# Optimization experiments

Measured on AMD Instinct MI355X. Metric: run time of the kernel, lower is better.

The kernel has to match this reference:

```python
import math
import jax, jax.numpy as jnp
import numpy as np
from jax import lax

B, CIN, COUT, K, SDIM, H, W = 8, 64, 64, 3, 512, 256, 256
EPS = 1e-8

def setup_inputs() -> dict:
    key = jax.random.key(0)
    k1, k2, k3, k4 = jax.random.split(key, 4)
    return {
        "input": jax.random.normal(k1, (B, CIN, H, W), dtype=jnp.float32),
        "style": jax.random.normal(k2, (B, SDIM), dtype=jnp.float32),
        "weight": jax.random.normal(k3, (1, COUT, CIN, K, K), dtype=jnp.float32),
        "mod_weight": jax.random.normal(k4, (CIN, SDIM), dtype=jnp.float32),
        "mod_bias": jnp.ones((CIN,), dtype=jnp.float32),
    }

def reference(input, style, weight, mod_weight, mod_bias):
    b, cin, h, w = input.shape
    cout, k = weight.shape[1], weight.shape[3]
    scale = 1.0 / math.sqrt(cin * k * k)          # equalized-lr conv scale
    mod_scale = 1.0 / math.sqrt(mod_weight.shape[1])  # EqualLinear fan-in scale
    # style modulation: (B, Cin)
    s = jnp.einsum('bs,cs->bc', style, mod_weight) * mod_scale + mod_bias
    # modulated per-sample weights: (B, Cout, Cin, K, K)
    wmod = scale * weight * s[:, None, :, None, None]
    # demodulation over (Cin, K, K)
    demod = lax.rsqrt(jnp.sum(wmod * wmod, axis=(2, 3, 4)) + EPS)
    wmod = wmod * demod[:, :, None, None, None]
    # grouped conv with groups = batch
    x = input.reshape(1, b * cin, h, w)
    wg = wmod.reshape(b * cout, cin, k, k)
    pad = k // 2
    out = lax.conv_general_dilated(
        x, wg, window_strides=(1, 1), padding=[(pad, pad), (pad, pad)],
        dimension_numbers=('NCHW', 'OIHW', 'NCHW'), feature_group_count=b)
    return out.reshape(b, cout, h, w)
```

## Files before the change

### kernel.cpp

```cpp
#include <hip/hip_runtime.h>
#include <hip/hip_bf16.h>


#define CIN   64
#define COUT  64
#define SDIM  512

typedef short bf16x8 __attribute__((ext_vector_type(8)));
typedef float f32x4  __attribute__((ext_vector_type(4)));
typedef unsigned short u16;
typedef unsigned short us8 __attribute__((ext_vector_type(8)));

static __device__ __forceinline__ u16 f2bf(float f) {
    union { float f; unsigned u; } v; v.f = f;
    unsigned r = v.u + 0x7FFF + ((v.u >> 16) & 1);
    return (u16)(r >> 16);
}
static __device__ __forceinline__ float getc(const float4& f, int k) {
    return k == 0 ? f.x : k == 1 ? f.y : k == 2 ? f.z : f.w;
}

__global__ void k_style(const float* __restrict__ style, const float* __restrict__ mw,
                        const float* __restrict__ mb, float* __restrict__ s_out) {
    int b = blockIdx.x;
    int t = threadIdx.x;
    int cin = t & 63, seg = t >> 6;
    const float4* st = (const float4*)(style + (size_t)b * SDIM) + seg * 32;
    const float4* w  = (const float4*)(mw + (size_t)cin * SDIM) + seg * 32;
    float acc = 0.f;
#pragma unroll 8
    for (int i = 0; i < 32; i++) {
        float4 a = st[i], bb = w[i];
        acc += a.x * bb.x + a.y * bb.y + a.z * bb.z + a.w * bb.w;
    }
    __shared__ float red[4][64];
    red[seg][cin] = acc;
    __syncthreads();
    if (seg == 0) {
        float v = red[0][cin] + red[1][cin] + red[2][cin] + red[3][cin];
        s_out[b * CIN + cin] = v * 0.04419417382415922f + mb[cin];
    }
}

__global__ void k_wdemod(const float* __restrict__ weight, const float* __restrict__ s,
                         u16* __restrict__ wA) {
    int bid = blockIdx.x;
    int b = bid >> 6, co = bid & 63;
    int cin = threadIdx.x;
    float sv = s[b * CIN + cin] * (1.0f / 24.0f);
    const float* wp = weight + ((size_t)co * CIN + cin) * 9;
    float w[9]; float sq = 0.f;
#pragma unroll
    for (int k = 0; k < 9; k++) { w[k] = wp[k] * sv; sq += w[k] * w[k]; }
#pragma unroll
    for (int off = 32; off; off >>= 1) sq += __shfl_xor(sq, off, 64);
    float dm = 1.0f / sqrtf(sq + 1e-8f);
    u16* dst = wA + (((size_t)b * COUT + co) * 9) * 64 + cin;
#pragma unroll
    for (int k = 0; k < 9; k++) dst[k * 64] = f2bf(w[k] * dm);
}

__global__ __launch_bounds__(256, 2) void k_conv2(
        const float* __restrict__ in, const u16* __restrict__ wA,
        float* __restrict__ out) {
    __shared__ __align__(16) u16 Xs[6 * 72 * 64];

    int raw = blockIdx.x;
    int swz = (raw & 7) * 256 + (raw >> 3);
    int b = swz >> 8, r = swz & 255;
    int y0 = (r >> 2) * 4, x0 = (r & 3) * 64;
    int tid = threadIdx.x;

    const float* inb = in + (size_t)b * (CIN * 65536);
    for (int u = tid; u < 864; u += 256) {
        int cing = u & 7;
        int g = u >> 3;
        int x4 = g % 18, yy = g / 18;
        int y = y0 + yy - 1;
        int x = x0 - 4 + x4 * 4;
        float4 f[8];
        if (y >= 0 && y < 256 && x >= 0 && x < 253) {
            const float* p = inb + (size_t)(cing * 8) * 65536 + (size_t)y * 256 + x;
#pragma unroll
            for (int j = 0; j < 8; j++) f[j] = *(const float4*)(p + (size_t)j * 65536);
        } else {
#pragma unroll
            for (int j = 0; j < 8; j++) f[j] = make_float4(0.f, 0.f, 0.f, 0.f);
        }
#pragma unroll
        for (int k = 0; k < 4; k++) {
            union { us8 v; unsigned w[4]; } pk;
#pragma unroll
            for (int p2 = 0; p2 < 4; p2++) {
                __hip_bfloat162 h = __float22bfloat162_rn(
                    make_float2(getc(f[2 * p2], k), getc(f[2 * p2 + 1], k)));
                unsigned wv_; __builtin_memcpy(&wv_, &h, 4);
                pk.w[p2] = wv_;
            }
            int xl = x4 * 4 + k;
            unsigned bo = (unsigned)(((yy * 72 + xl) * 64 + cing * 8) * 2)
                        ^ ((unsigned)(xl & 7) << 4);
            *(us8*)((char*)Xs + bo) = pk.v;
        }
    }
    __syncthreads();

    int wv = tid >> 6, l = tid & 63, lr = l & 15, lg = l >> 4;
    const u16* wAb = wA + (size_t)b * (COUT * 9 * 64);

    f32x4 acc[4][4];
#pragma unroll
    for (int ct = 0; ct < 4; ct++)
#pragma unroll
        for (int xt = 0; xt < 4; xt++) acc[ct][xt] = (f32x4){0.f, 0.f, 0.f, 0.f};

#pragma unroll
    for (int kk = 0; kk < 9; kk++) {
        const int dh = kk / 3, dw = kk % 3;
        const int yl = wv + dh;
#pragma unroll
        for (int half = 0; half < 2; half++) {
            bf16x8 afr[4], bfr[4];
#pragma unroll
            for (int ct = 0; ct < 4; ct++)
                afr[ct] = *(const bf16x8*)(wAb + ((size_t)(ct * 16 + lr) * 9 + kk) * 64
                                           + half * 32 + lg * 8);
#pragma unroll
            for (int xt = 0; xt < 4; xt++) {
                int xl = xt * 16 + lr + dw + 3;
                unsigned bo = (unsigned)(((yl * 72 + xl) * 64 + half * 32 + lg * 8) * 2)
                            ^ ((unsigned)(xl & 7) << 4);
                bfr[xt] = *(const bf16x8*)((const char*)Xs + bo);
            }
#pragma unroll
            for (int ct = 0; ct < 4; ct++)
#pragma unroll
                for (int xt = 0; xt < 4; xt++)
                    acc[ct][xt] = __builtin_amdgcn_mfma_f32_16x16x32_bf16(
                        afr[ct], bfr[xt], acc[ct][xt], 0, 0, 0);
        }
    }

    __syncthreads();
    float* ep = ((float*)Xs) + wv * (16 * 68);
    float* ob = out + ((size_t)b * COUT) * 65536 + (size_t)(y0 + wv) * 256 + x0;
    int c = l >> 2, xq = l & 3;
#pragma unroll
    for (int ct = 0; ct < 4; ct++) {
#pragma unroll
        for (int xt = 0; xt < 4; xt++)
#pragma unroll
            for (int q = 0; q < 4; q++)
                ep[(lg * 4 + q) * 68 + xt * 16 + lr] = acc[ct][xt][q];
        asm volatile("s_waitcnt lgkmcnt(0)" ::: "memory");
#pragma unroll
        for (int k = 0; k < 4; k++) {
            float4 v = *(const float4*)(ep + c * 68 + k * 16 + xq * 4);
            *(float4*)(ob + (size_t)(ct * 16 + c) * 65536 + k * 16 + xq * 4) = v;
        }
    }
}

extern "C" void kernel_launch(void* const* d_in, const int* in_sizes, int n_in,
                              void* d_out, int out_size, void* d_ws, size_t ws_size,
                              hipStream_t stream) {
    const float* input      = (const float*)d_in[0];
    const float* style      = (const float*)d_in[1];
    const float* weight     = (const float*)d_in[2];
    const float* mod_weight = (const float*)d_in[3];
    const float* mod_bias   = (const float*)d_in[4];
    float* out = (float*)d_out;

    char* ws = (char*)d_ws;
    u16*   wA = (u16*)ws;
    float* s  = (float*)(ws + 589824);

    k_style <<<8,    256, 0, stream>>>(style, mod_weight, mod_bias, s);
    k_wdemod<<<512,  64,  0, stream>>>(weight, s, wA);
    k_conv2 <<<2048, 256, 0, stream>>>(input, wA, out);
}
```

Measured before the change: 324.4 us.

## Split waves over output-channel and row halves, preload weights into registers

Each wave now handles 32 output channels by 2 rows, where before it handled 64 channels by 1 row. The wave's 36 weight fragments (2 channel tiles by 9 taps by 2 halves) are loaded from global memory into registers before the input staging, instead of being reloaded inside the MFMA loop. This removes repeated global weight loads from the inner loop and overlaps them with the shared-memory fill. In exchange, register pressure rises (about 144 VGPRs for weights plus 64 for accumulators) under launch bounds of 2 blocks, which could spill.

```diff
diff --git a/kernel.cpp b/kernel.cpp
--- a/kernel.cpp
+++ b/kernel.cpp
@@ -70,6 +70,20 @@
     int b = swz >> 8, r = swz & 255;
     int y0 = (r >> 2) * 4, x0 = (r & 3) * 64;
     int tid = threadIdx.x;
+    int wv = tid >> 6, l = tid & 63, lr = l & 15, lg = l >> 4;
+    int wy = wv & 1, cy = wv >> 1;
+
+    const u16* wAb = wA + (size_t)b * (COUT * 9 * 64);
+    bf16x8 wfr[2][9][2];
+#pragma unroll
+    for (int ct = 0; ct < 2; ct++)
+#pragma unroll
+        for (int kk = 0; kk < 9; kk++)
+#pragma unroll
+            for (int half = 0; half < 2; half++)
+                wfr[ct][kk][half] = *(const bf16x8*)(
+                    wAb + ((size_t)((cy * 2 + ct) * 16 + lr) * 9 + kk) * 64
+                        + half * 32 + lg * 8);
 
     const float* inb = in + (size_t)b * (CIN * 65536);
     for (int u = tid; u < 864; u += 256) {
@@ -105,60 +119,64 @@
     }
     __syncthreads();
 
-    int wv = tid >> 6, l = tid & 63, lr = l & 15, lg = l >> 4;
-    const u16* wAb = wA + (size_t)b * (COUT * 9 * 64);
-
-    f32x4 acc[4][4];
+    f32x4 acc[2][2][4];
 #pragma unroll
-    for (int ct = 0; ct < 4; ct++)
+    for (int yy = 0; yy < 2; yy++)
 #pragma unroll
-        for (int xt = 0; xt < 4; xt++) acc[ct][xt] = (f32x4){0.f, 0.f, 0.f, 0.f};
+        for (int ct = 0; ct < 2; ct++)
+#pragma unroll
+            for (int xt = 0; xt < 4; xt++) acc[yy][ct][xt] = (f32x4){0.f, 0.f, 0.f, 0.f};
 
 #pragma unroll
     for (int kk = 0; kk < 9; kk++) {
         const int dh = kk / 3, dw = kk % 3;
-        const int yl = wv + dh;
 #pragma unroll
         for (int half = 0; half < 2; half++) {
-            bf16x8 afr[4], bfr[4];
+            bf16x8 bfr[2][4];
 #pragma unroll
-            for (int ct = 0; ct < 4; ct++)
-                afr[ct] = *(const bf16x8*)(wAb + ((size_t)(ct * 16 + lr) * 9 + kk) * 64
-                                           + half * 32 + lg * 8);
+            for (int yy = 0; yy < 2; yy++) {
+                const int yl = wy * 2 + yy + dh;
 #pragma unroll
-            for (int xt = 0; xt < 4; xt++) {
-                int xl = xt * 16 + lr + dw + 3;
-                unsigned bo = (unsigned)(((yl * 72 + xl) * 64 + half * 32 + lg * 8) * 2)
-                            ^ ((unsigned)(xl & 7) << 4);
-                bfr[xt] = *(const bf16x8*)((const char*)Xs + bo);
+                for (int xt = 0; xt < 4; xt++) {
+                    int xl = xt * 16 + lr + dw + 3;
+                    unsigned bo = (unsigned)(((yl * 72 + xl) * 64 + half * 32 + lg * 8) * 2)
+                                ^ ((unsigned)(xl & 7) << 4);
+                    bfr[yy][xt] = *(const bf16x8*)((const char*)Xs + bo);
+                }
             }
 #pragma unroll
-            for (int ct = 0; ct < 4; ct++)
+            for (int ct = 0; ct < 2; ct++)
 #pragma unroll
-                for (int xt = 0; xt < 4; xt++)
-                    acc[ct][xt] = __builtin_amdgcn_mfma_f32_16x16x32_bf16(
-                        afr[ct], bfr[xt], acc[ct][xt], 0, 0, 0);
+                for (int yy = 0; yy < 2; yy++)
+#pragma unroll
+                    for (int xt = 0; xt < 4; xt++)
+                        acc[yy][ct][xt] = __builtin_amdgcn_mfma_f32_16x16x32_bf16(
+                            wfr[ct][kk][half], bfr[yy][xt], acc[yy][ct][xt], 0, 0, 0);
         }
     }
 
     __syncthreads();
     float* ep = ((float*)Xs) + wv * (16 * 68);
-    float* ob = out + ((size_t)b * COUT) * 65536 + (size_t)(y0 + wv) * 256 + x0;
     int c = l >> 2, xq = l & 3;
+    float* obase = out + (size_t)b * COUT * 65536;
 #pragma unroll
-    for (int ct = 0; ct < 4; ct++) {
+    for (int ct = 0; ct < 2; ct++)
 #pragma unroll
-        for (int xt = 0; xt < 4; xt++)
+        for (int yy = 0; yy < 2; yy++) {
 #pragma unroll
-            for (int q = 0; q < 4; q++)
-                ep[(lg * 4 + q) * 68 + xt * 16 + lr] = acc[ct][xt][q];
-        asm volatile("s_waitcnt lgkmcnt(0)" ::: "memory");
+            for (int xt = 0; xt < 4; xt++)
 #pragma unroll
-        for (int k = 0; k < 4; k++) {
-            float4 v = *(const float4*)(ep + c * 68 + k * 16 + xq * 4);
-            *(float4*)(ob + (size_t)(ct * 16 + c) * 65536 + k * 16 + xq * 4) = v;
+                for (int q = 0; q < 4; q++)
+                    ep[(lg * 4 + q) * 68 + xt * 16 + lr] = acc[yy][ct][xt][q];
+            asm volatile("s_waitcnt lgkmcnt(0)" ::: "memory");
+            float* ob = obase + (size_t)(cy * 32 + ct * 16 + c) * 65536
+                      + (size_t)(y0 + wy * 2 + yy) * 256 + x0;
+#pragma unroll
+            for (int k = 0; k < 4; k++) {
+                float4 v = *(const float4*)(ep + c * 68 + k * 16 + xq * 4);
+                *(float4*)(ob + k * 16 + xq * 4) = v;
+            }
         }
-    }
 }
 
 extern "C" void kernel_launch(void* const* d_in, const int* in_sizes, int n_in,
```

Result: slower. 333.1 us (+2.7%).
